# Performance work log

Hardware: AMD Instinct MI355X
Metric: run time of the kernel (lower is better)

## Reference

```python
import jax, jax.numpy as jnp
import numpy as np

N, E, B = 50000, 100000, 512   # nodes, edges, graphs
H, F_NODE, F_EDGE, T_OUT = 64, 16, 8, 1
T = 3                           # message-passing steps


def setup_inputs() -> dict:
    key = jax.random.key(0)
    ks = jax.random.split(key, 18)

    def w(k, shape, fan_in):
        return jax.random.normal(k, shape, dtype=jnp.float32) / np.sqrt(fan_in)

    return {
        "node_features": jax.random.normal(ks[0], (N, F_NODE), dtype=jnp.float32),
        "edge_features": jax.random.normal(ks[1], (E, F_EDGE), dtype=jnp.float32),
        "Esrc": jax.random.randint(ks[2], (E,), 0, N, dtype=jnp.int32),
        "Etgt": jax.random.randint(ks[3], (E,), 0, N, dtype=jnp.int32),
        "batch": jnp.sort(jax.random.randint(ks[4], (N,), 0, B, dtype=jnp.int32)),
        # input linear: node_features -> hidden
        "Win": w(ks[5], (H, F_NODE), F_NODE),
        "bin_": jnp.zeros((H,), jnp.float32),
        # edge encoder MLP: edge_features -> hidden -> hidden*hidden
        "We1": w(ks[6], (H, F_EDGE), F_EDGE),
        "be1": jnp.zeros((H,), jnp.float32),
        "We2": w(ks[7], (H * H, H), H),
        "be2": jnp.zeros((H * H,), jnp.float32),
        # GRU cell (shared across T steps)
        "Wih": w(ks[8], (3 * H, H), H),
        "bih": jnp.zeros((3 * H,), jnp.float32),
        "Whh": w(ks[9], (3 * H, H), H),
        "bhh": jnp.zeros((3 * H,), jnp.float32),
        # output linear: hidden -> target_features
        "Wout": w(ks[10], (T_OUT, H), H),
        "bout": jnp.zeros((T_OUT,), jnp.float32),
    }


def _gru(x, h, Wih, bih, Whh, bhh):
    gi = x @ Wih.T + bih            # [N, 3H]
    gh = h @ Whh.T + bhh
    i_r, i_z, i_n = jnp.split(gi, 3, axis=-1)
    h_r, h_z, h_n = jnp.split(gh, 3, axis=-1)
    r = jax.nn.sigmoid(i_r + h_r)
    z = jax.nn.sigmoid(i_z + h_z)
    n = jnp.tanh(i_n + r * h_n)
    return (1.0 - z) * n + z * h


def reference(node_features, edge_features, Esrc, Etgt, batch,
              Win, bin_, We1, be1, We2, be2,
              Wih, bih, Whh, bhh, Wout, bout):
    # Edge encoder MLP -> per-edge [H, H] message matrix (ENN style)
    eh = jax.nn.relu(edge_features @ We1.T + be1)          # [E, H]
    edge_data = (eh @ We2.T + be2).reshape(E, H, H)        # [E, H, H]

    x = node_features @ Win.T + bin_                       # [N, H]

    for _ in range(T):  # small fixed layer count
        msg = jnp.einsum('eij,ej->ei', edge_data, x[Esrc])  # per-edge matvec
        agg = jax.ops.segment_sum(msg, Etgt, num_segments=N)
        x = _gru(agg, x, Wih, bih, Whh, bhh)

    out = x @ Wout.T + bout                                # [N, 1]
    pooled = jax.ops.segment_sum(out, batch, num_segments=B)  # [B, 1]
    return pooled
```

## Files before the change

kernel.cpp:

```cpp
#include <hip/hip_runtime.h>
#include <hip/hip_fp16.h>

#define NN 50000
#define NE 100000
#define NB 512
#define NBLK_SCAN 196

typedef _Float16 f16x8 __attribute__((ext_vector_type(8)));
typedef float f32x4   __attribute__((ext_vector_type(4)));
typedef float f32x16  __attribute__((ext_vector_type(16)));

__device__ __forceinline__ float sigm(float v) { return 1.0f / (1.0f + __expf(-v)); }
__device__ __forceinline__ float tanh_fast(float v) {
    float e = __expf(-2.0f * fabsf(v));
    float t = (1.0f - e) / (1.0f + e);
    return v < 0.f ? -t : t;
}

#define PREP_GRID 38636

__global__ __launch_bounds__(256) void prep_kernel(
    const float* __restrict__ nf, const float* __restrict__ Win,
    const float* __restrict__ bin_, float* __restrict__ x, __half* __restrict__ xh,
    const float* __restrict__ ef, const float* __restrict__ We1,
    const float* __restrict__ be1, __half* __restrict__ ehh,
    const float* __restrict__ We2, const float* __restrict__ be2,
    __half* __restrict__ Bp,
    const float* __restrict__ Wih, const float* __restrict__ Whh,
    __half* __restrict__ WG)
{
    const int b = blockIdx.x;
    const int tid = threadIdx.x;
    if (b < 12500) {
        int idx = b * 256 + tid;
        int n = idx >> 6, h = idx & 63;
        float acc = bin_[h];
        #pragma unroll
        for (int f = 0; f < 16; f++) acc += nf[n * 16 + f] * Win[h * 16 + f];
        x[idx] = acc;
        xh[idx] = __float2half(acc);
    } else if (b < 37500) {
        int idx = (b - 12500) * 256 + tid;
        int e = idx >> 6, k = idx & 63;
        float acc = be1[k];
        #pragma unroll
        for (int f = 0; f < 8; f++) acc += ef[e * 8 + f] * We1[k * 8 + f];
        ehh[idx] = __float2half(fmaxf(acc, 0.0f));
    } else if (b < 38540) {
        int idx = (b - 37500) * 256 + tid;
        int ii = idx & 7;
        int l  = (idx >> 3) & 63;
        int nt = (idx >> 9) & 1;
        int kt = idx >> 10;
        int n  = nt * 32 + (l & 31);
        int p  = kt * 16 + ((l >> 5) << 3) + ii;
        float v;
        if (p < 4096) {
            v = We2[((size_t)(n * 64 + (p >> 6))) * 64 + (p & 63)];
        } else {
            v = be2[n * 64 + (p - 4096)];
        }
        Bp[idx] = __float2half(v);
    } else {
        int idx = (b - 38540) * 256 + tid;
        int kk = idx & 31;
        int n  = (idx >> 5) & 15;
        int nt = (idx >> 9) % 24;
        int kt = (idx >> 9) / 24;
        int k = kt * 32 + kk;
        int col192 = (nt % 12) * 16 + n;
        int gate = col192 >> 6, h = col192 & 63;
        const float* src = (nt < 12) ? Wih : Whh;
        WG[idx] = __float2half(src[((size_t)(gate * 64 + h)) * 64 + k]);
    }
}


__global__ __launch_bounds__(256) void hist_kernel(
    const int* __restrict__ Etgt, int* __restrict__ cnt)
{
    int e = blockIdx.x * 256 + threadIdx.x;
    if (e < NE) atomicAdd(&cnt[Etgt[e]], 1);
}

__device__ __forceinline__ int block_excl_scan(int v, int tid, int* lds)
{
    int lane = tid & 63, w = tid >> 6;
    int incl = v;
    #pragma unroll
    for (int d = 1; d < 64; d <<= 1) {
        int u = __shfl_up(incl, d, 64);
        if (lane >= d) incl += u;
    }
    if (lane == 63) lds[w] = incl;
    __syncthreads();
    if (tid == 0) {
        int a = lds[0], b = lds[1], c = lds[2];
        lds[4] = 0; lds[5] = a; lds[6] = a + b; lds[7] = a + b + c;
    }
    __syncthreads();
    return incl - v + lds[4 + w];
}

__global__ __launch_bounds__(256) void scanA_kernel(
    const int* __restrict__ cnt, int* __restrict__ bsum)
{
    __shared__ int s4[4];
    int tid = threadIdx.x;
    int idx = blockIdx.x * 256 + tid;
    int v = (idx < NN) ? cnt[idx] : 0;
    #pragma unroll
    for (int d = 1; d < 64; d <<= 1) v += __shfl_xor(v, d, 64);
    if ((tid & 63) == 0) s4[tid >> 6] = v;
    __syncthreads();
    if (tid == 0) bsum[blockIdx.x] = s4[0] + s4[1] + s4[2] + s4[3];
}

__global__ __launch_bounds__(256) void scanB_kernel(
    const int* __restrict__ bsum, int* __restrict__ bscan, int* __restrict__ off)
{
    __shared__ int lds[8];
    int tid = threadIdx.x;
    int v = (tid < NBLK_SCAN) ? bsum[tid] : 0;
    int ex = block_excl_scan(v, tid, lds);
    if (tid < NBLK_SCAN) bscan[tid] = ex;
    if (tid == NBLK_SCAN) off[NN] = ex;
}

__global__ __launch_bounds__(256) void scanC_kernel(
    const int* __restrict__ cnt, const int* __restrict__ bscan,
    int* __restrict__ off, int* __restrict__ wpos)
{
    __shared__ int lds[8];
    int tid = threadIdx.x;
    int idx = blockIdx.x * 256 + tid;
    int v = (idx < NN) ? cnt[idx] : 0;
    int ex = block_excl_scan(v, tid, lds) + bscan[blockIdx.x];
    if (idx < NN) { off[idx] = ex; wpos[idx] = ex; }
}

__global__ __launch_bounds__(256) void scatter_kernel(
    const int* __restrict__ Etgt, int* __restrict__ wpos,
    int* __restrict__ inv, int* __restrict__ tgt_sorted)
{
    int e = blockIdx.x * 256 + threadIdx.x;
    if (e < NE) {
        int t = Etgt[e];
        int p = atomicAdd(&wpos[t], 1);
        inv[e] = p;
        tgt_sorted[p] = t;
    }
}

__global__ __launch_bounds__(256, 4) void msg_kernel(
    const __half* __restrict__ xh, const __half* __restrict__ ehh,
    const __half* __restrict__ Bp,
    const int* __restrict__ Esrc, const int* __restrict__ inv,
    float* __restrict__ msgf)
{
    __shared__ __align__(16) __half xs[128][72];
    __shared__ __align__(16) __half bbuf[2][4096];
    __shared__ int inv_s[128];
    const int tid = threadIdx.x;
    const int e0 = blockIdx.x * 128;
    const int w = tid >> 6, lane = tid & 63;
    const int l31 = lane & 31, khalf = lane >> 5;

    {
        const int r = tid >> 1, part = tid & 1;
        const int e = e0 + r;
        const bool ok = (e < NE);
        const int src = ok ? Esrc[e] : 0;
        if (part == 0) inv_s[r] = ok ? inv[e] : 0;
        const uint4* xsrc = (const uint4*)(xh + (size_t)src * 64 + part * 32);
        __half* dst = &xs[r][part * 32];
        #pragma unroll
        for (int i = 0; i < 4; i++) {
            uint4 v = ok ? xsrc[i] : make_uint4(0, 0, 0, 0);
            *(uint4*)(dst + i * 8) = v;
        }
    }

    {
        const uint4* s = (const uint4*)Bp;
        uint4 v0 = s[tid], v1 = s[256 + tid];
        ((uint4*)bbuf[0])[tid] = v0;
        ((uint4*)bbuf[0])[256 + tid] = v1;
    }

    const int eMine = e0 + w * 32 + l31;
    __half2 ehc2[4][4];
    if (eMine < NE) {
        #pragma unroll
        for (int kt = 0; kt < 4; kt++) {
            union { uint4 u; __half2 h[4]; } u0;
            u0.u = *(const uint4*)(ehh + (size_t)eMine * 64 + kt * 16 + khalf * 8);
            #pragma unroll
            for (int q = 0; q < 4; q++) ehc2[kt][q] = u0.h[q];
        }
    } else {
        __half2 z = __halves2half2(__float2half(0.f), __float2half(0.f));
        #pragma unroll
        for (int kt = 0; kt < 4; kt++)
            #pragma unroll
            for (int q = 0; q < 4; q++) ehc2[kt][q] = z;
    }

    f32x16 acc[2];
    #pragma unroll
    for (int nt = 0; nt < 2; nt++)
        #pragma unroll
        for (int q = 0; q < 16; q++) acc[nt][q] = 0.f;

    __syncthreads();

    int cur = 0;
    #pragma unroll 1
    for (int j = 0; j < 64; j++) {
        const uint4* s = (const uint4*)(Bp + (size_t)(j + 1) * 4096);
        uint4 p0 = s[tid];
        uint4 p1 = s[256 + tid];

        const __half xv = xs[w * 32 + l31][j];
        const __half2 xb = __half2half2(xv);

        #pragma unroll
        for (int kt = 0; kt < 4; kt++) {
            union { __half2 h[4]; f16x8 v; } u;
            #pragma unroll
            for (int q = 0; q < 4; q++) u.h[q] = __hmul2(xb, ehc2[kt][q]);
            #pragma unroll
            for (int nt = 0; nt < 2; nt++) {
                f16x8 bf = *(const f16x8*)(&bbuf[cur][(kt * 2 + nt) * 512 + lane * 8]);
                acc[nt] = __builtin_amdgcn_mfma_f32_32x32x16_f16(
                    u.v, bf, acc[nt], 0, 0, 0);
            }
        }

        uint4* d = (uint4*)bbuf[cur ^ 1];
        d[tid] = p0;
        d[256 + tid] = p1;
        __syncthreads();
        cur ^= 1;
    }

    #pragma unroll
    for (int ktl = 0; ktl < 4; ktl++) {
        f16x8 af = *(const f16x8*)(&xs[w * 32 + l31][ktl * 16 + khalf * 8]);
        #pragma unroll
        for (int nt = 0; nt < 2; nt++) {
            f16x8 bf = *(const f16x8*)(&bbuf[cur][(ktl * 2 + nt) * 512 + lane * 8]);
            acc[nt] = __builtin_amdgcn_mfma_f32_32x32x16_f16(
                af, bf, acc[nt], 0, 0, 0);
        }
    }

    #pragma unroll
    for (int nt = 0; nt < 2; nt++) {
        #pragma unroll
        for (int r = 0; r < 16; r++) {
            const int erow = w * 32 + (r & 3) + 8 * (r >> 2) + 4 * khalf;
            const int e = e0 + erow;
            if (e < NE)
                msgf[(size_t)inv_s[erow] * 64 + nt * 32 + l31] = acc[nt][r];
        }
    }
}

__global__ __launch_bounds__(256, 4) void gru_kernel(
    const float* __restrict__ msgf, const int* __restrict__ off,
    const int* __restrict__ tgt_sorted,
    float* __restrict__ x, __half* __restrict__ xh,
    const __half* __restrict__ WG,
    const float* __restrict__ bih, const float* __restrict__ bhh,
    const float* __restrict__ Wout, const float* __restrict__ bout,
    const int* __restrict__ batch, float* __restrict__ out, int dopool)
{
    __shared__ float aggs[64][68];
    const int tid = threadIdx.x;
    const int w = tid >> 6, lane = tid & 63, m = lane & 15, quad = lane >> 4;
    const int nb0 = blockIdx.x * 64;

    {
        float* a = &aggs[0][0];
        #pragma unroll
        for (int i = 0; i < 17; i++) a[i * 256 + tid] = 0.f;
    }
    __syncthreads();

    const int hi = (nb0 + 64 < NN) ? nb0 + 64 : NN;
    {
        const int r0 = off[nb0], r1 = off[hi];
        for (int p = r0 + w; p < r1; p += 4) {
            float v = msgf[(size_t)p * 64 + lane];
            int t = tgt_sorted[p];
            atomicAdd(&aggs[t - nb0][lane], v);
        }
    }
    __syncthreads();

    const int nbase = nb0 + w * 16;
    const int anode = nbase + m;
    const bool aok = (anode < NN);

    f16x8 a_agg[2], a_x[2];
    #pragma unroll
    for (int kt = 0; kt < 2; kt++) {
        const int koff = kt * 32 + quad * 8;
        {
            const float* ap = &aggs[w * 16 + m][koff];
            float4 f0 = *(const float4*)ap;
            float4 f1 = *(const float4*)(ap + 4);
            union { __half2 h[4]; f16x8 v; } u;
            u.h[0] = __floats2half2_rn(f0.x, f0.y);
            u.h[1] = __floats2half2_rn(f0.z, f0.w);
            u.h[2] = __floats2half2_rn(f1.x, f1.y);
            u.h[3] = __floats2half2_rn(f1.z, f1.w);
            a_agg[kt] = u.v;
        }
        if (aok) {
            a_x[kt] = *(const f16x8*)(xh + (size_t)anode * 64 + koff);
        } else {
            f16x8 z;
            #pragma unroll
            for (int i = 0; i < 8; i++) z[i] = (_Float16)0;
            a_x[kt] = z;
        }
    }

    float pdr0 = 0.f, pdr1 = 0.f, pdr2 = 0.f, pdr3 = 0.f;

    #pragma unroll
    for (int t = 0; t < 4; t++) {
        f32x4 accg[6];
        #pragma unroll
        for (int g = 0; g < 6; g++)
            #pragma unroll
            for (int q = 0; q < 4; q++) accg[g][q] = 0.f;

        #pragma unroll
        for (int g = 0; g < 6; g++) {
            const int nt = g * 4 + t;
            #pragma unroll
            for (int kt = 0; kt < 2; kt++) {
                f16x8 b = *(const f16x8*)(WG + (size_t)(kt * 24 + nt) * 512 + m * 32 + quad * 8);
                accg[g] = __builtin_amdgcn_mfma_f32_16x16x32_f16(
                    (g < 3) ? a_agg[kt] : a_x[kt], b, accg[g], 0, 0, 0);
            }
        }

        const int h = t * 16 + m;
        const float bir = bih[h], biz = bih[64 + h], bin = bih[128 + h];
        const float bhr = bhh[h], bhz = bhh[64 + h], bhn = bhh[128 + h];
        const float wo = dopool ? Wout[h] : 0.f;
        #pragma unroll
        for (int r = 0; r < 4; r++) {
            const int nd = nbase + quad * 4 + r;
            if (nd >= NN) continue;
            float ir  = accg[0][r] + bir;
            float iz  = accg[1][r] + biz;
            float in_ = accg[2][r] + bin;
            float hr  = accg[3][r] + bhr;
            float hz  = accg[4][r] + bhz;
            float hn  = accg[5][r] + bhn;
            float rg = sigm(ir + hr);
            float z  = sigm(iz + hz);
            float n  = tanh_fast(in_ + rg * hn);
            float xold = x[(size_t)nd * 64 + h];
            float xn = (1.0f - z) * n + z * xold;
            x[(size_t)nd * 64 + h] = xn;
            xh[(size_t)nd * 64 + h] = __float2half(xn);
            float c = xn * wo;
            if (r == 0) pdr0 += c; else if (r == 1) pdr1 += c;
            else if (r == 2) pdr2 += c; else pdr3 += c;
        }
    }

    if (dopool) {
        float pdr[4] = {pdr0, pdr1, pdr2, pdr3};
        #pragma unroll
        for (int r = 0; r < 4; r++) {
            float v = pdr[r];
            v += __shfl_xor(v, 1, 16);
            v += __shfl_xor(v, 2, 16);
            v += __shfl_xor(v, 4, 16);
            v += __shfl_xor(v, 8, 16);
            if (m == 0) {
                const int nd = nbase + quad * 4 + r;
                if (nd < NN) atomicAdd(out + batch[nd], v + bout[0]);
            }
        }
    }
}

extern "C" void kernel_launch(void* const* d_in, const int* in_sizes, int n_in,
                              void* d_out, int out_size, void* d_ws, size_t ws_size,
                              hipStream_t stream)
{
    const float* nf   = (const float*)d_in[0];
    const float* ef   = (const float*)d_in[1];
    const int*   Esrc = (const int*)  d_in[2];
    const int*   Etgt = (const int*)  d_in[3];
    const int*   bat  = (const int*)  d_in[4];
    const float* Win  = (const float*)d_in[5];
    const float* bin_ = (const float*)d_in[6];
    const float* We1  = (const float*)d_in[7];
    const float* be1  = (const float*)d_in[8];
    const float* We2  = (const float*)d_in[9];
    const float* be2  = (const float*)d_in[10];
    const float* Wih  = (const float*)d_in[11];
    const float* bih  = (const float*)d_in[12];
    const float* Whh  = (const float*)d_in[13];
    const float* bhh  = (const float*)d_in[14];
    const float* Wout = (const float*)d_in[15];
    const float* bout = (const float*)d_in[16];

    char* ws = (char*)d_ws;
    float*  x          = (float*)(ws);
    float*  msgf       = (float*)(ws + 12800000);
    __half* xh         = (__half*)(ws + 38400000);
    __half* ehh        = (__half*)(ws + 44800000);
    __half* Bp         = (__half*)(ws + 57600000);
    __half* WG         = (__half*)(ws + 58132480);
    int*    cnt        = (int*)   (ws + 58181632);
    int*    off        = (int*)   (ws + 58381648);
    int*    wpos       = (int*)   (ws + 58581664);
    int*    inv        = (int*)   (ws + 58781680);
    int*    tgt_sorted = (int*)   (ws + 59181680);
    int*    bsum       = (int*)   (ws + 59581680);
    int*    bscan      = (int*)   (ws + 59582704);

    hipMemsetAsync(d_out, 0, NB * sizeof(float), stream);
    hipMemsetAsync(cnt, 0, (NN + 1) * sizeof(int), stream);

    prep_kernel<<<PREP_GRID, 256, 0, stream>>>(
        nf, Win, bin_, x, xh, ef, We1, be1, ehh, We2, be2, Bp, Wih, Whh, WG);

    hist_kernel<<<(NE + 255) / 256, 256, 0, stream>>>(Etgt, cnt);
    scanA_kernel<<<NBLK_SCAN, 256, 0, stream>>>(cnt, bsum);
    scanB_kernel<<<1, 256, 0, stream>>>(bsum, bscan, off);
    scanC_kernel<<<NBLK_SCAN, 256, 0, stream>>>(cnt, bscan, off, wpos);
    scatter_kernel<<<(NE + 255) / 256, 256, 0, stream>>>(Etgt, wpos, inv, tgt_sorted);

    for (int t = 0; t < 3; t++) {
        msg_kernel<<<(NE + 127) / 128, 256, 0, stream>>>(xh, ehh, Bp, Esrc, inv, msgf);
        gru_kernel<<<(NN + 63) / 64, 256, 0, stream>>>(
            msgf, off, tgt_sorted, x, xh, WG, bih, bhh,
            Wout, bout, bat, (float*)d_out, (t == 2) ? 1 : 0);
    }
}
```

Before: 568.2 us.

## Split segment-sum out of GRU kernel into CSR gather kernel, prefetch GRU weights

Moves the per-node aggregation of edge messages out of the GRU kernel into a separate segsum kernel. Each node now sums its contiguous CSR range of messages in registers and writes an fp16 aggregate, which replaces the LDS atomicAdd loop and removes the tgt_sorted array. The GRU kernel loads the fp16 aggregate directly, prefetches all weight fragments and old x values before the MFMAs, and raises its occupancy hint. The cost is an extra kernel launch and an extra global round-trip for the aggregate on each step.

Result: faster. 518.1 us (-8.8%).

```diff
diff --git a/kernel.cpp b/kernel.cpp
--- a/kernel.cpp
+++ b/kernel.cpp
@@ -140,15 +140,12 @@
 }
 
 __global__ __launch_bounds__(256) void scatter_kernel(
-    const int* __restrict__ Etgt, int* __restrict__ wpos,
-    int* __restrict__ inv, int* __restrict__ tgt_sorted)
+    const int* __restrict__ Etgt, int* __restrict__ wpos, int* __restrict__ inv)
 {
     int e = blockIdx.x * 256 + threadIdx.x;
     if (e < NE) {
-        int t = Etgt[e];
-        int p = atomicAdd(&wpos[t], 1);
+        int p = atomicAdd(&wpos[Etgt[e]], 1);
         inv[e] = p;
-        tgt_sorted[p] = t;
     }
 }
 
@@ -267,39 +264,37 @@
     }
 }
 
-__global__ __launch_bounds__(256, 4) void gru_kernel(
+__global__ __launch_bounds__(256) void segsum_kernel(
     const float* __restrict__ msgf, const int* __restrict__ off,
-    const int* __restrict__ tgt_sorted,
+    __half* __restrict__ aggh)
+{
+    const int tid = threadIdx.x;
+    const int n = blockIdx.x * 16 + (tid >> 4);
+    const int c4 = (tid & 15) * 4;
+    if (n >= NN) return;
+    const int r0 = off[n], r1 = off[n + 1];
+    float4 acc = make_float4(0.f, 0.f, 0.f, 0.f);
+    for (int p = r0; p < r1; ++p) {
+        float4 v = *(const float4*)(msgf + (size_t)p * 64 + c4);
+        acc.x += v.x; acc.y += v.y; acc.z += v.z; acc.w += v.w;
+    }
+    union { __half2 h[2]; unsigned long long u; } pk;
+    pk.h[0] = __floats2half2_rn(acc.x, acc.y);
+    pk.h[1] = __floats2half2_rn(acc.z, acc.w);
+    *(unsigned long long*)(aggh + (size_t)n * 64 + c4) = pk.u;
+}
+
+__global__ __launch_bounds__(256, 6) void gru_kernel(
+    const __half* __restrict__ aggh,
     float* __restrict__ x, __half* __restrict__ xh,
     const __half* __restrict__ WG,
     const float* __restrict__ bih, const float* __restrict__ bhh,
     const float* __restrict__ Wout, const float* __restrict__ bout,
     const int* __restrict__ batch, float* __restrict__ out, int dopool)
 {
-    __shared__ float aggs[64][68];
     const int tid = threadIdx.x;
     const int w = tid >> 6, lane = tid & 63, m = lane & 15, quad = lane >> 4;
-    const int nb0 = blockIdx.x * 64;
-
-    {
-        float* a = &aggs[0][0];
-        #pragma unroll
-        for (int i = 0; i < 17; i++) a[i * 256 + tid] = 0.f;
-    }
-    __syncthreads();
-
-    const int hi = (nb0 + 64 < NN) ? nb0 + 64 : NN;
-    {
-        const int r0 = off[nb0], r1 = off[hi];
-        for (int p = r0 + w; p < r1; p += 4) {
-            float v = msgf[(size_t)p * 64 + lane];
-            int t = tgt_sorted[p];
-            atomicAdd(&aggs[t - nb0][lane], v);
-        }
-    }
-    __syncthreads();
-
-    const int nbase = nb0 + w * 16;
+    const int nbase = blockIdx.x * 64 + w * 16;
     const int anode = nbase + m;
     const bool aok = (anode < NN);
 
@@ -307,24 +302,14 @@
     #pragma unroll
     for (int kt = 0; kt < 2; kt++) {
         const int koff = kt * 32 + quad * 8;
-        {
-            const float* ap = &aggs[w * 16 + m][koff];
-            float4 f0 = *(const float4*)ap;
-            float4 f1 = *(const float4*)(ap + 4);
-            union { __half2 h[4]; f16x8 v; } u;
-            u.h[0] = __floats2half2_rn(f0.x, f0.y);
-            u.h[1] = __floats2half2_rn(f0.z, f0.w);
-            u.h[2] = __floats2half2_rn(f1.x, f1.y);
-            u.h[3] = __floats2half2_rn(f1.z, f1.w);
-            a_agg[kt] = u.v;
-        }
         if (aok) {
-            a_x[kt] = *(const f16x8*)(xh + (size_t)anode * 64 + koff);
+            a_agg[kt] = *(const f16x8*)(aggh + (size_t)anode * 64 + koff);
+            a_x[kt]   = *(const f16x8*)(xh   + (size_t)anode * 64 + koff);
         } else {
             f16x8 z;
             #pragma unroll
             for (int i = 0; i < 8; i++) z[i] = (_Float16)0;
-            a_x[kt] = z;
+            a_agg[kt] = z; a_x[kt] = z;
         }
     }
 
@@ -332,6 +317,22 @@
 
     #pragma unroll
     for (int t = 0; t < 4; t++) {
+        const int h = t * 16 + m;
+
+        f16x8 bfr[12];
+        #pragma unroll
+        for (int g = 0; g < 6; g++)
+            #pragma unroll
+            for (int kt = 0; kt < 2; kt++)
+                bfr[g * 2 + kt] = *(const f16x8*)(
+                    WG + (size_t)(kt * 24 + g * 4 + t) * 512 + m * 32 + quad * 8);
+        float xold[4];
+        #pragma unroll
+        for (int r = 0; r < 4; r++) {
+            const int nd = nbase + quad * 4 + r;
+            xold[r] = (nd < NN) ? x[(size_t)nd * 64 + h] : 0.f;
+        }
+
         f32x4 accg[6];
         #pragma unroll
         for (int g = 0; g < 6; g++)
@@ -339,17 +340,12 @@
             for (int q = 0; q < 4; q++) accg[g][q] = 0.f;
 
         #pragma unroll
-        for (int g = 0; g < 6; g++) {
-            const int nt = g * 4 + t;
-            #pragma unroll
-            for (int kt = 0; kt < 2; kt++) {
-                f16x8 b = *(const f16x8*)(WG + (size_t)(kt * 24 + nt) * 512 + m * 32 + quad * 8);
+        for (int g = 0; g < 6; g++)
+            #pragma unroll
+            for (int kt = 0; kt < 2; kt++)
                 accg[g] = __builtin_amdgcn_mfma_f32_16x16x32_f16(
-                    (g < 3) ? a_agg[kt] : a_x[kt], b, accg[g], 0, 0, 0);
-            }
-        }
-
-        const int h = t * 16 + m;
+                    (g < 3) ? a_agg[kt] : a_x[kt], bfr[g * 2 + kt], accg[g], 0, 0, 0);
+
         const float bir = bih[h], biz = bih[64 + h], bin = bih[128 + h];
         const float bhr = bhh[h], bhz = bhh[64 + h], bhn = bhh[128 + h];
         const float wo = dopool ? Wout[h] : 0.f;
@@ -366,8 +362,7 @@
             float rg = sigm(ir + hr);
             float z  = sigm(iz + hz);
             float n  = tanh_fast(in_ + rg * hn);
-            float xold = x[(size_t)nd * 64 + h];
-            float xn = (1.0f - z) * n + z * xold;
+            float xn = (1.0f - z) * n + z * xold[r];
             x[(size_t)nd * 64 + h] = xn;
             xh[(size_t)nd * 64 + h] = __float2half(xn);
             float c = xn * wo;
@@ -416,19 +411,19 @@
     const float* bout = (const float*)d_in[16];
 
     char* ws = (char*)d_ws;
-    float*  x          = (float*)(ws);
-    float*  msgf       = (float*)(ws + 12800000);
-    __half* xh         = (__half*)(ws + 38400000);
-    __half* ehh        = (__half*)(ws + 44800000);
-    __half* Bp         = (__half*)(ws + 57600000);
-    __half* WG         = (__half*)(ws + 58132480);
-    int*    cnt        = (int*)   (ws + 58181632);
-    int*    off        = (int*)   (ws + 58381648);
-    int*    wpos       = (int*)   (ws + 58581664);
-    int*    inv        = (int*)   (ws + 58781680);
-    int*    tgt_sorted = (int*)   (ws + 59181680);
-    int*    bsum       = (int*)   (ws + 59581680);
-    int*    bscan      = (int*)   (ws + 59582704);
+    float*  x     = (float*)(ws);
+    float*  msgf  = (float*)(ws + 12800000);
+    __half* xh    = (__half*)(ws + 38400000);
+    __half* ehh   = (__half*)(ws + 44800000);
+    __half* Bp    = (__half*)(ws + 57600000);
+    __half* WG    = (__half*)(ws + 58132480);
+    int*    cnt   = (int*)   (ws + 58181632);
+    int*    off   = (int*)   (ws + 58381648);
+    int*    wpos  = (int*)   (ws + 58581664);
+    int*    inv   = (int*)   (ws + 58781680);
+    __half* aggh  = (__half*)(ws + 59181680);
+    int*    bsum  = (int*)   (ws + 65581680);
+    int*    bscan = (int*)   (ws + 65582704);
 
     hipMemsetAsync(d_out, 0, NB * sizeof(float), stream);
     hipMemsetAsync(cnt, 0, (NN + 1) * sizeof(int), stream);
@@ -440,12 +435,13 @@
     scanA_kernel<<<NBLK_SCAN, 256, 0, stream>>>(cnt, bsum);
     scanB_kernel<<<1, 256, 0, stream>>>(bsum, bscan, off);
     scanC_kernel<<<NBLK_SCAN, 256, 0, stream>>>(cnt, bscan, off, wpos);
-    scatter_kernel<<<(NE + 255) / 256, 256, 0, stream>>>(Etgt, wpos, inv, tgt_sorted);
+    scatter_kernel<<<(NE + 255) / 256, 256, 0, stream>>>(Etgt, wpos, inv);
 
     for (int t = 0; t < 3; t++) {
         msg_kernel<<<(NE + 127) / 128, 256, 0, stream>>>(xh, ehh, Bp, Esrc, inv, msgf);
+        segsum_kernel<<<(NN + 15) / 16, 256, 0, stream>>>(msgf, off, aggh);
         gru_kernel<<<(NN + 63) / 64, 256, 0, stream>>>(
-            msgf, off, tgt_sorted, x, xh, WG, bih, bhh,
+            aggh, x, xh, WG, bih, bhh,
             Wout, bout, bat, (float*)d_out, (t == 2) ? 1 : 0);
     }
 }
```
